# Performance work log

Hardware: AMD Instinct MI355X
Metric: run time of the kernel (lower is better)

Reference implementation:

```python
import jax, jax.numpy as jnp
import numpy as np

N = 100000   # nodes
E = 3200000  # edges per graph
DP, DA, DF, H, C = 3, 11, 32, 4, 8  # d_p, d_a, d_feat, heads, per-head dim
NEG_SLOPE = 0.2


def gat_conv(x, edge_index, W, att_src, att_dst, bias):
    """PyG GATConv with concat heads and default add_self_loops=True.
    x: [N, DF]; edge_index: [2, E] (row0=src, row1=dst); W: [DF, H*C];
    att_src/att_dst: [H, C]; bias: [H*C]. Returns [N, H*C]."""
    n = x.shape[0]
    loops = jnp.arange(n, dtype=edge_index.dtype)
    src = jnp.concatenate([edge_index[0], loops])
    dst = jnp.concatenate([edge_index[1], loops])
    h = (x @ W).reshape(n, H, C)                       # [N,H,C]
    a_s = jnp.sum(h * att_src[None], axis=-1)          # [N,H]
    a_d = jnp.sum(h * att_dst[None], axis=-1)          # [N,H]
    e = jax.nn.leaky_relu(a_s[src] + a_d[dst], NEG_SLOPE)  # [Etot,H]
    m = jax.ops.segment_max(e, dst, num_segments=n)        # stable softmax per dst
    ex = jnp.exp(e - m[dst])
    den = jax.ops.segment_sum(ex, dst, num_segments=n)
    alpha = ex / den[dst]                               # [Etot,H]
    out = jax.ops.segment_sum(h[src] * alpha[..., None], dst, num_segments=n)
    return out.reshape(n, H * C) + bias


def setup_inputs() -> dict:
    key = jax.random.key(0)
    ks = jax.random.split(key, 32)
    p = lambda k, shp: (jax.random.normal(k, shp, dtype=jnp.float32) * 0.1)
    inp = {
        "F_p_raw": jax.random.normal(ks[0], (N, DP), dtype=jnp.float32),
        "F_a_raw": jax.random.normal(ks[1], (N, DA), dtype=jnp.float32),
        "edge_index_s": jax.random.randint(ks[2], (2, E), 0, N),
        "edge_index_p": jax.random.randint(ks[3], (2, E), 0, N),
        "edge_index_a": jax.random.randint(ks[4], (2, E), 0, N),
        # align linears
        "Wp": p(ks[5], (DP, DF)), "bp": p(ks[6], (DF,)),
        "Wa": p(ks[7], (DA, DF)), "ba": p(ks[8], (DF,)),
        "Ws": p(ks[9], (DP + DA, DF)), "bs": p(ks[10], (DF,)),
        # GAT params per graph
        "Wg_s": p(ks[11], (DF, H * C)), "asrc_s": p(ks[12], (H, C)), "adst_s": p(ks[13], (H, C)), "bg_s": p(ks[14], (H * C,)),
        "Wg_p": p(ks[15], (DF, H * C)), "asrc_p": p(ks[16], (H, C)), "adst_p": p(ks[17], (H, C)), "bg_p": p(ks[18], (H * C,)),
        "Wg_a": p(ks[19], (DF, H * C)), "asrc_a": p(ks[20], (H, C)), "adst_a": p(ks[21], (H, C)), "bg_a": p(ks[22], (H * C,)),
        # fuse MLP
        "W1": p(ks[23], (3 * DF, DF)), "b1": p(ks[24], (DF,)),
        "W2": p(ks[25], (DF, DF)), "b2": p(ks[26], (DF,)),
    }
    return inp


def reference(F_p_raw, F_a_raw, edge_index_s, edge_index_p, edge_index_a,
              Wp, bp, Wa, ba, Ws, bs,
              Wg_s, asrc_s, adst_s, bg_s,
              Wg_p, asrc_p, adst_p, bg_p,
              Wg_a, asrc_a, adst_a, bg_a,
              W1, b1, W2, b2):
    f_s = jnp.concatenate([F_p_raw, F_a_raw], axis=-1) @ Ws + bs
    f_p = F_p_raw @ Wp + bp
    f_a = F_a_raw @ Wa + ba
    h_s = jax.nn.elu(gat_conv(f_s, edge_index_s, Wg_s, asrc_s, adst_s, bg_s))
    h_p = jax.nn.elu(gat_conv(f_p, edge_index_p, Wg_p, asrc_p, adst_p, bg_p))
    h_a = jax.nn.elu(gat_conv(f_a, edge_index_a, Wg_a, asrc_a, adst_a, bg_a))
    h = jnp.concatenate([h_s, h_p, h_a], axis=-1)
    h = jax.nn.relu(h @ W1 + b1)
    return h @ W2 + b2
```

## Files before the change

### kernel.cpp

```cpp
#include <hip/hip_runtime.h>
#include <hip/hip_bf16.h>
#include <stdint.h>

typedef __hip_bfloat16 bf16;

__device__ __forceinline__ float b2f(bf16 v){ return __bfloat162float(v); }

__device__ __forceinline__ uint16_t f2b(float x){
  uint32_t u = __float_as_uint(x);
  return (uint16_t)((u + 0x7FFFu + ((u >> 16) & 1u)) >> 16);
}

#define DSTS_PER_BKT 128
#define BKT_SHIFT 7
#define CAP 6144
#define BIN_IT 32
#define MAXB 1024
#define ROWS_PER_WAVE (DSTS_PER_BKT / 4)
#define CURPAD 16

struct CvtTab {
  const void* src[24];
  int n[24];
  int off[24];
};

__global__ __launch_bounds__(256) void k_detect(const void* __restrict__ sample,
                                                int* __restrict__ flag)
{
  __shared__ int bad;
  if (threadIdx.x == 0) bad = 0;
  __syncthreads();
  const unsigned short* u = (const unsigned short*)sample;
  int lbad = 0;
  for (int k = threadIdx.x; k < 1024; k += 256) {
    unsigned short b = u[k];
    unsigned e = (b >> 7) & 0xFFu;
    if (e >= 141u || (e <= 90u && (b & 0x7FFFu) != 0)) lbad = 1;
  }
  if (lbad) atomicOr(&bad, 1);
  __syncthreads();
  if (threadIdx.x == 0) flag[0] = (bad == 0) ? 1 : 0;
}

__global__ __launch_bounds__(256) void k_convert(CvtTab tab, const int* __restrict__ flag,
                                                 float* __restrict__ dst, int total)
{
  const bool isb = (*flag) != 0;
  for (int t = blockIdx.x * 256 + threadIdx.x; t < total; t += gridDim.x * 256) {
    int a = 0;
    while (a < 23 && t >= tab.off[a] + tab.n[a]) ++a;
    int j = t - tab.off[a];
    float v = isb ? b2f(((const bf16*)tab.src[a])[j])
                  : ((const float*)tab.src[a])[j];
    dst[t] = v;
  }
}

__global__ __launch_bounds__(256) void k_node(
  const float* __restrict__ cFp, const float* __restrict__ cFa,
  const float* __restrict__ cWp, const float* __restrict__ cbp,
  const float* __restrict__ cWa, const float* __restrict__ cba,
  const float* __restrict__ cWs, const float* __restrict__ cbs,
  const float* __restrict__ cWg0, const float* __restrict__ cAs0, const float* __restrict__ cAd0,
  const float* __restrict__ cWg1, const float* __restrict__ cAs1, const float* __restrict__ cAd1,
  const float* __restrict__ cWg2, const float* __restrict__ cAs2, const float* __restrict__ cAd2,
  uint32_t* __restrict__ hgb, uint16_t* __restrict__ asb, float* __restrict__ a_d,
  float* __restrict__ den, float* __restrict__ agg, int N)
{
  __shared__ float sWs[14*32];
  __shared__ float sWp[3*32];
  __shared__ float sWa[11*32];
  __shared__ float sb[3][32];
  __shared__ float sWg[3][32*32];
  __shared__ float sA[3][2][32];
  const int tid = threadIdx.x;
  for (int t = tid; t < 14*32; t += 256) sWs[t] = cWs[t];
  for (int t = tid; t < 3*32;  t += 256) sWp[t] = cWp[t];
  for (int t = tid; t < 11*32; t += 256) sWa[t] = cWa[t];
  if (tid < 32) {
    sb[0][tid] = cbs[tid]; sb[1][tid] = cbp[tid]; sb[2][tid] = cba[tid];
    sA[0][0][tid] = cAs0[tid]; sA[0][1][tid] = cAd0[tid];
    sA[1][0][tid] = cAs1[tid]; sA[1][1][tid] = cAd1[tid];
    sA[2][0][tid] = cAs2[tid]; sA[2][1][tid] = cAd2[tid];
  }
  for (int t = tid; t < 32*32; t += 256) {
    sWg[0][t] = cWg0[t]; sWg[1][t] = cWg1[t]; sWg[2][t] = cWg2[t];
  }
  __syncthreads();

  const int i = blockIdx.x * 256 + tid;
  if (i >= N) return;

  float xp[3], xa[11];
  #pragma unroll
  for (int k = 0; k < 3; ++k)  xp[k] = cFp[i*3 + k];
  #pragma unroll
  for (int k = 0; k < 11; ++k) xa[k] = cFa[i*11 + k];

  for (int g = 0; g < 3; ++g) {
    float f[32];
    if (g == 0) {
      #pragma unroll
      for (int j = 0; j < 32; ++j) {
        float acc = sb[0][j];
        #pragma unroll
        for (int k = 0; k < 3; ++k)  acc += xp[k] * sWs[k*32 + j];
        #pragma unroll
        for (int k = 0; k < 11; ++k) acc += xa[k] * sWs[(3+k)*32 + j];
        f[j] = acc;
      }
    } else if (g == 1) {
      #pragma unroll
      for (int j = 0; j < 32; ++j) {
        float acc = sb[1][j];
        #pragma unroll
        for (int k = 0; k < 3; ++k) acc += xp[k] * sWp[k*32 + j];
        f[j] = acc;
      }
    } else {
      #pragma unroll
      for (int j = 0; j < 32; ++j) {
        float acc = sb[2][j];
        #pragma unroll
        for (int k = 0; k < 11; ++k) acc += xa[k] * sWa[k*32 + j];
        f[j] = acc;
      }
    }

    const float* Wg = sWg[g];
    float hv[32];
    #pragma unroll
    for (int j = 0; j < 32; ++j) {
      float acc = 0.f;
      #pragma unroll
      for (int k = 0; k < 32; ++k) acc += f[k] * Wg[k*32 + j];
      hv[j] = acc;
    }

    float asv[4], adv[4], exv[4];
    #pragma unroll
    for (int h = 0; h < 4; ++h) {
      float s0 = 0.f, s1 = 0.f;
      #pragma unroll
      for (int c = 0; c < 8; ++c) {
        s0 += hv[h*8 + c] * sA[g][0][h*8 + c];
        s1 += hv[h*8 + c] * sA[g][1][h*8 + c];
      }
      asv[h] = s0; adv[h] = s1;
      float e = s0 + s1;
      e = e > 0.f ? e : 0.2f * e;
      exv[h] = __expf(e);
    }

    const size_t row = (size_t)g * N + i;
    uint32_t* hp = hgb + row * 16;
    #pragma unroll
    for (int q = 0; q < 4; ++q) {
      uint4 u;
      u.x = (uint32_t)f2b(hv[q*8+0]) | ((uint32_t)f2b(hv[q*8+1]) << 16);
      u.y = (uint32_t)f2b(hv[q*8+2]) | ((uint32_t)f2b(hv[q*8+3]) << 16);
      u.z = (uint32_t)f2b(hv[q*8+4]) | ((uint32_t)f2b(hv[q*8+5]) << 16);
      u.w = (uint32_t)f2b(hv[q*8+6]) | ((uint32_t)f2b(hv[q*8+7]) << 16);
      *(uint4*)(hp + q*4) = u;
    }
    *(ushort4*)(asb + row * 4) =
        make_ushort4(f2b(asv[0]), f2b(asv[1]), f2b(asv[2]), f2b(asv[3]));

    float4* agp = (float4*)(agg + row * 32);
    #pragma unroll
    for (int q = 0; q < 8; ++q) {
      float ex = exv[q >> 1];
      agp[q] = make_float4(ex*hv[q*4+0], ex*hv[q*4+1], ex*hv[q*4+2], ex*hv[q*4+3]);
    }
    *(float4*)(a_d + row*4) = make_float4(adv[0], adv[1], adv[2], adv[3]);
    *(float4*)(den + row*4) = make_float4(exv[0], exv[1], exv[2], exv[3]);
  }
}

__global__ __launch_bounds__(256) void k_hist(
  const int* __restrict__ ei0, const int* __restrict__ ei1, const int* __restrict__ ei2,
  int* __restrict__ gb_hist, int NBPG, int E)
{
  const int g = blockIdx.y;
  const int* __restrict__ ei = (g == 0) ? ei0 : (g == 1 ? ei1 : ei2);
  __shared__ int hist[MAXB];
  for (int t = threadIdx.x; t < NBPG; t += 256) hist[t] = 0;
  __syncthreads();
  const int base = blockIdx.x * (256 * BIN_IT);
  #pragma unroll
  for (int k = 0; k < BIN_IT; ++k) {
    int idx = base + k * 256 + threadIdx.x;
    if (idx < E) atomicAdd(&hist[ei[E + idx] >> BKT_SHIFT], 1);
  }
  __syncthreads();
  for (int t = threadIdx.x; t < NBPG; t += 256)
    if (hist[t]) atomicAdd(&gb_hist[g * NBPG + t], hist[t]);
}

#define SCAN_IPT 16
__global__ __launch_bounds__(256) void k_bscan(
  const int* __restrict__ gb_hist, int* __restrict__ boff, int* __restrict__ cur, int nb)
{
  __shared__ int s[256];
  const int base = threadIdx.x * SCAN_IPT;
  int v[SCAN_IPT]; int sum = 0;
  #pragma unroll
  for (int k = 0; k < SCAN_IPT; ++k) {
    int i = base + k; int x = (i < nb) ? gb_hist[i] : 0; v[k] = x; sum += x;
  }
  s[threadIdx.x] = sum;
  __syncthreads();
  for (int d = 1; d < 256; d <<= 1) {
    int t = (threadIdx.x >= d) ? s[threadIdx.x - d] : 0;
    __syncthreads();
    s[threadIdx.x] += t;
    __syncthreads();
  }
  int run = s[threadIdx.x] - sum;
  #pragma unroll
  for (int k = 0; k < SCAN_IPT; ++k) {
    int i = base + k;
    if (i < nb) { boff[i] = run; cur[(size_t)i * CURPAD] = run; run += v[k]; }
  }
  if (threadIdx.x == 255) boff[nb] = s[255];
}

__global__ __launch_bounds__(256) void k_bin(
  const int* __restrict__ ei0, const int* __restrict__ ei1, const int* __restrict__ ei2,
  int* __restrict__ cur, int* __restrict__ bins, int NBPG, int E)
{
  const int g = blockIdx.y;
  const int* __restrict__ ei = (g == 0) ? ei0 : (g == 1 ? ei1 : ei2);
  __shared__ int sp[256 * BIN_IT];
  __shared__ int hist[MAXB];
  __shared__ int soff[MAXB];
  __shared__ int grun[MAXB];
  __shared__ int s[256];
  const int tid = threadIdx.x;
  for (int t = tid; t < NBPG; t += 256) hist[t] = 0;
  __syncthreads();
  const int base = blockIdx.x * (256 * BIN_IT);

  int pk[BIN_IT];
  #pragma unroll
  for (int k = 0; k < BIN_IT; ++k) {
    int idx = base + k * 256 + tid;
    if (idx < E) {
      int d = ei[E + idx];
      int b = d >> BKT_SHIFT;
      int loc = atomicAdd(&hist[b], 1);
      pk[k] = (b << 20) | (loc << 7) | (d & (DSTS_PER_BKT - 1));
    } else pk[k] = -1;
  }
  __syncthreads();

  {
    const int sbase = tid * 4;
    int v[4]; int sum = 0;
    #pragma unroll
    for (int j = 0; j < 4; ++j) {
      int i = sbase + j; int x = (i < NBPG) ? hist[i] : 0; v[j] = x; sum += x;
    }
    s[tid] = sum;
    __syncthreads();
    for (int d = 1; d < 256; d <<= 1) {
      int t = (tid >= d) ? s[tid - d] : 0;
      __syncthreads();
      s[tid] += t;
      __syncthreads();
    }
    int run = s[tid] - sum;
    #pragma unroll
    for (int j = 0; j < 4; ++j) {
      int i = sbase + j;
      if (i < NBPG) { soff[i] = run; run += v[j]; }
    }
  }
  for (int t = tid; t < NBPG; t += 256) {
    int c = hist[t];
    grun[t] = c ? atomicAdd(&cur[(size_t)(g * NBPG + t) * CURPAD], c) : 0;
  }
  __syncthreads();

  #pragma unroll
  for (int k = 0; k < BIN_IT; ++k) {
    int p = pk[k];
    if (p >= 0) {
      int idx = base + k * 256 + tid;
      int src = ei[idx];
      int b   = p >> 20;
      int loc = (p >> 7) & 0x1FFF;
      int dl  = p & (DSTS_PER_BKT - 1);
      sp[soff[b] + loc] = (dl << 17) | src;
    }
  }
  __syncthreads();

  const int wave = tid >> 6, lane = tid & 63;
  for (int b = wave; b < NBPG; b += 4) {
    const int c  = hist[b];
    const int gb_ = grun[b];
    const int ls = soff[b];
    for (int i = lane; i < c; i += 64)
      bins[gb_ + i] = sp[ls + i];
  }
}

__global__ __launch_bounds__(256) void k_vgather(
  const int* __restrict__ boff, const int* __restrict__ bins,
  const uint32_t* __restrict__ hgb, const uint16_t* __restrict__ asb,
  const float* __restrict__ a_d,
  float* __restrict__ den, float* __restrict__ agg, int NBPG, int N)
{
  __shared__ int sorted[CAP];
  __shared__ int soff[DSTS_PER_BKT + 1];
  __shared__ int scnt[DSTS_PER_BKT];
  __shared__ int sscan[DSTS_PER_BKT];
  const int g  = blockIdx.y;
  const int b  = blockIdx.x;
  const int gb = g * NBPG + b;
  const int s0 = boff[gb];
  const int n  = boff[gb + 1] - s0;
  const int tid = threadIdx.x;
  const int wave = tid >> 6;
  const int lane = tid & 63;
  const int sub  = lane >> 4;
  const int l16  = lane & 15;
  const int h    = l16 >> 2;
  const size_t gbase = (size_t)g * N;
  const int dst0 = b * DSTS_PER_BKT;

  for (int cbase = 0; cbase < n; cbase += CAP) {
    const int m = min(CAP, n - cbase);
    if (tid < DSTS_PER_BKT) scnt[tid] = 0;
    __syncthreads();
    for (int i = tid; i < m; i += 256)
      atomicAdd(&scnt[(bins[s0 + cbase + i] >> 17) & (DSTS_PER_BKT - 1)], 1);
    __syncthreads();
    if (tid < DSTS_PER_BKT) sscan[tid] = scnt[tid];
    __syncthreads();
    for (int d = 1; d < DSTS_PER_BKT; d <<= 1) {
      int t = 0;
      if (tid < DSTS_PER_BKT && tid >= d) t = sscan[tid - d];
      __syncthreads();
      if (tid < DSTS_PER_BKT) sscan[tid] += t;
      __syncthreads();
    }
    if (tid < DSTS_PER_BKT) {
      int ex = sscan[tid] - scnt[tid];
      soff[tid] = ex;
      scnt[tid] = ex;
    }
    if (tid == 0) soff[DSTS_PER_BKT] = m;
    __syncthreads();
    for (int i = tid; i < m; i += 256) {
      int p = bins[s0 + cbase + i];
      int pos = atomicAdd(&scnt[(p >> 17) & (DSTS_PER_BKT - 1)], 1);
      sorted[pos] = p & 0x1FFFF;
    }
    __syncthreads();

    const int rbeg = wave * ROWS_PER_WAVE;
    for (int rl = rbeg; rl < rbeg + ROWS_PER_WAVE; ++rl) {
      const int dst = dst0 + rl;
      if (dst >= N) break;
      const int cs = soff[rl], ce = soff[rl + 1];
      const size_t row = gbase + dst;
      const float ad = a_d[row * 4 + h];
      float ax = 0.f, ay = 0.f, w = 0.f;
      for (int c = cs + sub; c < ce; c += 16) {
        const int i0 = c        < ce ? sorted[c]      : -1;
        const int i1 = (c + 4)  < ce ? sorted[c + 4]  : -1;
        const int i2 = (c + 8)  < ce ? sorted[c + 8]  : -1;
        const int i3 = (c + 12) < ce ? sorted[c + 12] : -1;
        const int p0 = i0 < 0 ? 0 : i0;
        const int p1 = i1 < 0 ? 0 : i1;
        const int p2 = i2 < 0 ? 0 : i2;
        const int p3 = i3 < 0 ? 0 : i3;
        const uint32_t u0 = hgb[(gbase + p0) * 16 + l16];
        const uint32_t u1 = hgb[(gbase + p1) * 16 + l16];
        const uint32_t u2 = hgb[(gbase + p2) * 16 + l16];
        const uint32_t u3 = hgb[(gbase + p3) * 16 + l16];
        const uint16_t t0 = asb[(gbase + p0) * 4 + h];
        const uint16_t t1 = asb[(gbase + p1) * 4 + h];
        const uint16_t t2 = asb[(gbase + p2) * 4 + h];
        const uint16_t t3 = asb[(gbase + p3) * 4 + h];
        float e0 = __uint_as_float((uint32_t)t0 << 16) + ad; e0 = e0 > 0.f ? e0 : 0.2f * e0;
        float e1 = __uint_as_float((uint32_t)t1 << 16) + ad; e1 = e1 > 0.f ? e1 : 0.2f * e1;
        float e2 = __uint_as_float((uint32_t)t2 << 16) + ad; e2 = e2 > 0.f ? e2 : 0.2f * e2;
        float e3 = __uint_as_float((uint32_t)t3 << 16) + ad; e3 = e3 > 0.f ? e3 : 0.2f * e3;
        const float w0 = i0 >= 0 ? __expf(e0) : 0.f;
        const float w1 = i1 >= 0 ? __expf(e1) : 0.f;
        const float w2 = i2 >= 0 ? __expf(e2) : 0.f;
        const float w3 = i3 >= 0 ? __expf(e3) : 0.f;
        ax += w0 * __uint_as_float(u0 << 16);
        ay += w0 * __uint_as_float(u0 & 0xFFFF0000u);
        ax += w1 * __uint_as_float(u1 << 16);
        ay += w1 * __uint_as_float(u1 & 0xFFFF0000u);
        ax += w2 * __uint_as_float(u2 << 16);
        ay += w2 * __uint_as_float(u2 & 0xFFFF0000u);
        ax += w3 * __uint_as_float(u3 << 16);
        ay += w3 * __uint_as_float(u3 & 0xFFFF0000u);
        w += w0 + w1 + w2 + w3;
      }
      ax += __shfl_xor(ax, 16); ay += __shfl_xor(ay, 16); w += __shfl_xor(w, 16);
      ax += __shfl_xor(ax, 32); ay += __shfl_xor(ay, 32); w += __shfl_xor(w, 32);
      if (sub == 0) {
        float2* ap = (float2*)(agg + row * 32) + l16;
        float2 sv = *ap;
        sv.x += ax; sv.y += ay;
        *ap = sv;
        if ((l16 & 3) == 0) den[row * 4 + h] += w;
      }
    }
    __syncthreads();
  }
}

__global__ __launch_bounds__(256) void k_final(
  const float* __restrict__ den, const float* __restrict__ agg,
  const float* __restrict__ cbg0, const float* __restrict__ cbg1, const float* __restrict__ cbg2,
  const float* __restrict__ cW1, const float* __restrict__ cb1,
  const float* __restrict__ cW2, const float* __restrict__ cb2,
  const int* __restrict__ flag, void* __restrict__ out, int N)
{
  __shared__ float sW1[96*32];
  __shared__ float sW2[32*32];
  __shared__ float sb1[32], sb2[32], sbg[3][32];
  const int tid = threadIdx.x;
  for (int t = tid; t < 96*32; t += 256) sW1[t] = cW1[t];
  for (int t = tid; t < 32*32; t += 256) sW2[t] = cW2[t];
  if (tid < 32) {
    sb1[tid] = cb1[tid]; sb2[tid] = cb2[tid];
    sbg[0][tid] = cbg0[tid]; sbg[1][tid] = cbg1[tid]; sbg[2][tid] = cbg2[tid];
  }
  __syncthreads();

  const int i = blockIdx.x * 256 + tid;
  if (i >= N) return;

  float h96[96];
  #pragma unroll
  for (int g = 0; g < 3; ++g) {
    const size_t row = (size_t)g * N + i;
    float4 d4 = *(const float4*)(den + row * 4);
    float invs[4] = {1.f/d4.x, 1.f/d4.y, 1.f/d4.z, 1.f/d4.w};
    const float4* av = (const float4*)(agg + row * 32);
    #pragma unroll
    for (int q = 0; q < 8; ++q) {
      float4 a4 = av[q];
      float iv = invs[q >> 1];
      float vals[4] = {a4.x, a4.y, a4.z, a4.w};
      #pragma unroll
      for (int k = 0; k < 4; ++k) {
        float v = vals[k] * iv + sbg[g][q*4 + k];
        v = v > 0.f ? v : (__expf(v) - 1.f);
        h96[g*32 + q*4 + k] = v;
      }
    }
  }

  float h1[32];
  #pragma unroll
  for (int j = 0; j < 32; ++j) {
    float acc = sb1[j];
    #pragma unroll
    for (int k = 0; k < 96; ++k) acc += h96[k] * sW1[k*32 + j];
    h1[j] = acc > 0.f ? acc : 0.f;
  }

  const bool isb = (*flag) != 0;
  #pragma unroll
  for (int j = 0; j < 32; ++j) {
    float acc = sb2[j];
    #pragma unroll
    for (int k = 0; k < 32; ++k) acc += h1[k] * sW2[k*32 + j];
    if (isb) ((bf16*)out)[(size_t)i*32 + j] = __float2bfloat16(acc);
    else     ((float*)out)[(size_t)i*32 + j] = acc;
  }
}

extern "C" void kernel_launch(void* const* d_in, const int* in_sizes, int n_in,
                              void* d_out, int out_size, void* d_ws, size_t ws_size,
                              hipStream_t stream)
{
  const int N = in_sizes[0] / 3;
  const int E = in_sizes[2] / 2;
  const int NBPG = (N + DSTS_PER_BKT - 1) / DSTS_PER_BKT;
  const int nb = 3 * NBPG;

  float* ws  = (float*)d_ws;
  int* flag  = (int*)d_ws;
  float* cvt = ws + 64;

  static const int order[24] = {1, 0,
    5, 6, 7, 8, 9, 10,
    11, 12, 13, 14,
    15, 16, 17, 18,
    19, 20, 21, 22,
    23, 24, 25, 26};
  CvtTab tab;
  int off0 = 0;
  for (int a = 0; a < 24; ++a) {
    tab.src[a] = d_in[order[a]];
    tab.n[a]   = in_sizes[order[a]];
    tab.off[a] = off0;
    off0 += tab.n[a];
  }
  const int total = off0;

  float* P[24];
  for (int a = 0; a < 24; ++a) P[a] = cvt + tab.off[a];
  float *cFa = P[0],  *cFp = P[1];
  float *cWp = P[2],  *cbp = P[3],  *cWa = P[4],  *cba = P[5],  *cWs = P[6], *cbs = P[7];
  float *cWg0 = P[8],  *cAs0 = P[9],  *cAd0 = P[10], *cbg0 = P[11];
  float *cWg1 = P[12], *cAs1 = P[13], *cAd1 = P[14], *cbg1 = P[15];
  float *cWg2 = P[16], *cAs2 = P[17], *cAd2 = P[18], *cbg2 = P[19];
  float *cW1 = P[20], *cb1 = P[21], *cW2 = P[22], *cb2 = P[23];

  int pad = (4 - (total & 3)) & 3;
  float* big = cvt + total + pad;
  const size_t n3 = (size_t)3 * N;
  float* agg  = big;
  float* a_d  = agg + n3 * 32;
  float* den  = a_d + n3 * 4;
  uint32_t* hgb = (uint32_t*)(den + n3 * 4);
  uint16_t* asb = (uint16_t*)(hgb + n3 * 16);
  int* gb_hist = (int*)(asb + n3 * 4);
  int* boff    = gb_hist + nb;
  int* cur     = boff + nb + 1;
  int* bins    = cur + (size_t)nb * CURPAD + CURPAD;

  const int ebx = (E + 256 * BIN_IT - 1) / (256 * BIN_IT);

  k_detect<<<1, 256, 0, stream>>>(d_in[1], flag);
  k_convert<<<2048, 256, 0, stream>>>(tab, flag, cvt, total);
  k_node<<<(N + 255) / 256, 256, 0, stream>>>(
      cFp, cFa, cWp, cbp, cWa, cba, cWs, cbs,
      cWg0, cAs0, cAd0, cWg1, cAs1, cAd1, cWg2, cAs2, cAd2,
      hgb, asb, a_d, den, agg, N);

  hipMemsetAsync(gb_hist, 0, nb * sizeof(int), stream);

  dim3 ge((unsigned)ebx, 3, 1);
  k_hist<<<ge, 256, 0, stream>>>(
      (const int*)d_in[2], (const int*)d_in[3], (const int*)d_in[4], gb_hist, NBPG, E);
  k_bscan<<<1, 256, 0, stream>>>(gb_hist, boff, cur, nb);
  k_bin<<<ge, 256, 0, stream>>>(
      (const int*)d_in[2], (const int*)d_in[3], (const int*)d_in[4], cur, bins, NBPG, E);

  dim3 gg((unsigned)NBPG, 3, 1);
  k_vgather<<<gg, 256, 0, stream>>>(boff, bins, hgb, asb, a_d, den, agg, NBPG, N);

  k_final<<<(N + 255) / 256, 256, 0, stream>>>(
      den, agg, cbg0, cbg1, cbg2, cW1, cb1, cW2, cb2, flag, d_out, N);
}
```

Measured before the change: 499.4 us.

## Replace global histogram/scan binning with per-block local sort plus directory

Drops the global histogram, scan and atomic cursor passes, so no memset is needed either. Each edge block now sorts its 8192 edges by bucket in shared memory and writes them contiguously, along with a per-block offset directory. The gather kernel then reads one run per edge block for its bucket and scans the run lengths itself. This saves two launches and two passes over edges, at the cost of many small scattered reads (about 391 runs per bucket) and a larger directory in the gather kernel.

```diff
diff --git a/kernel.cpp b/kernel.cpp
--- a/kernel.cpp
+++ b/kernel.cpp
@@ -13,11 +13,12 @@
 
 #define DSTS_PER_BKT 128
 #define BKT_SHIFT 7
-#define CAP 6144
+#define CHUNKE 8192
+#define CAP 8192
 #define BIN_IT 32
 #define MAXB 1024
+#define NBLKMAX 512
 #define ROWS_PER_WAVE (DSTS_PER_BKT / 4)
-#define CURPAD 16
 
 struct CvtTab {
   const void* src[24];
@@ -178,69 +179,23 @@
   }
 }
 
-__global__ __launch_bounds__(256) void k_hist(
+__global__ __launch_bounds__(256) void k_bin2(
   const int* __restrict__ ei0, const int* __restrict__ ei1, const int* __restrict__ ei2,
-  int* __restrict__ gb_hist, int NBPG, int E)
+  int* __restrict__ dir, int* __restrict__ bins, int NBPG, int NBLK, int E)
 {
   const int g = blockIdx.y;
   const int* __restrict__ ei = (g == 0) ? ei0 : (g == 1 ? ei1 : ei2);
+  __shared__ int sp[CHUNKE];
   __shared__ int hist[MAXB];
-  for (int t = threadIdx.x; t < NBPG; t += 256) hist[t] = 0;
-  __syncthreads();
-  const int base = blockIdx.x * (256 * BIN_IT);
-  #pragma unroll
-  for (int k = 0; k < BIN_IT; ++k) {
-    int idx = base + k * 256 + threadIdx.x;
-    if (idx < E) atomicAdd(&hist[ei[E + idx] >> BKT_SHIFT], 1);
-  }
-  __syncthreads();
-  for (int t = threadIdx.x; t < NBPG; t += 256)
-    if (hist[t]) atomicAdd(&gb_hist[g * NBPG + t], hist[t]);
-}
-
-#define SCAN_IPT 16
-__global__ __launch_bounds__(256) void k_bscan(
-  const int* __restrict__ gb_hist, int* __restrict__ boff, int* __restrict__ cur, int nb)
-{
-  __shared__ int s[256];
-  const int base = threadIdx.x * SCAN_IPT;
-  int v[SCAN_IPT]; int sum = 0;
-  #pragma unroll
-  for (int k = 0; k < SCAN_IPT; ++k) {
-    int i = base + k; int x = (i < nb) ? gb_hist[i] : 0; v[k] = x; sum += x;
-  }
-  s[threadIdx.x] = sum;
-  __syncthreads();
-  for (int d = 1; d < 256; d <<= 1) {
-    int t = (threadIdx.x >= d) ? s[threadIdx.x - d] : 0;
-    __syncthreads();
-    s[threadIdx.x] += t;
-    __syncthreads();
-  }
-  int run = s[threadIdx.x] - sum;
-  #pragma unroll
-  for (int k = 0; k < SCAN_IPT; ++k) {
-    int i = base + k;
-    if (i < nb) { boff[i] = run; cur[(size_t)i * CURPAD] = run; run += v[k]; }
-  }
-  if (threadIdx.x == 255) boff[nb] = s[255];
-}
-
-__global__ __launch_bounds__(256) void k_bin(
-  const int* __restrict__ ei0, const int* __restrict__ ei1, const int* __restrict__ ei2,
-  int* __restrict__ cur, int* __restrict__ bins, int NBPG, int E)
-{
-  const int g = blockIdx.y;
-  const int* __restrict__ ei = (g == 0) ? ei0 : (g == 1 ? ei1 : ei2);
-  __shared__ int sp[256 * BIN_IT];
-  __shared__ int hist[MAXB];
-  __shared__ int soff[MAXB];
-  __shared__ int grun[MAXB];
+  __shared__ int soff[MAXB + 1];
   __shared__ int s[256];
   const int tid = threadIdx.x;
+  const int blk = blockIdx.x;
+  const int base = blk * CHUNKE;
+  const int m = min(CHUNKE, E - base);
+
   for (int t = tid; t < NBPG; t += 256) hist[t] = 0;
   __syncthreads();
-  const int base = blockIdx.x * (256 * BIN_IT);
 
   int pk[BIN_IT];
   #pragma unroll
@@ -256,11 +211,11 @@
   __syncthreads();
 
   {
-    const int sbase = tid * 4;
+    const int sb = tid * 4;
     int v[4]; int sum = 0;
     #pragma unroll
     for (int j = 0; j < 4; ++j) {
-      int i = sbase + j; int x = (i < NBPG) ? hist[i] : 0; v[j] = x; sum += x;
+      int i = sb + j; int x = (i < NBPG) ? hist[i] : 0; v[j] = x; sum += x;
     }
     s[tid] = sum;
     __syncthreads();
@@ -273,15 +228,15 @@
     int run = s[tid] - sum;
     #pragma unroll
     for (int j = 0; j < 4; ++j) {
-      int i = sbase + j;
+      int i = sb + j;
       if (i < NBPG) { soff[i] = run; run += v[j]; }
     }
-  }
-  for (int t = tid; t < NBPG; t += 256) {
-    int c = hist[t];
-    grun[t] = c ? atomicAdd(&cur[(size_t)(g * NBPG + t) * CURPAD], c) : 0;
-  }
-  __syncthreads();
+    if (tid == 255) soff[NBPG] = s[255];
+  }
+  __syncthreads();
+
+  for (int t = tid; t <= NBPG; t += 256)
+    dir[((size_t)(g * (NBPG + 1) + t)) * NBLK + blk] = soff[t];
 
   #pragma unroll
   for (int k = 0; k < BIN_IT; ++k) {
@@ -297,32 +252,25 @@
   }
   __syncthreads();
 
-  const int wave = tid >> 6, lane = tid & 63;
-  for (int b = wave; b < NBPG; b += 4) {
-    const int c  = hist[b];
-    const int gb_ = grun[b];
-    const int ls = soff[b];
-    for (int i = lane; i < c; i += 64)
-      bins[gb_ + i] = sp[ls + i];
-  }
+  const size_t ob = ((size_t)(g * NBLK + blk)) << 13;
+  for (int i = tid; i < m; i += 256) bins[ob + i] = sp[i];
 }
 
 __global__ __launch_bounds__(256) void k_vgather(
-  const int* __restrict__ boff, const int* __restrict__ bins,
+  const int* __restrict__ dir, const int* __restrict__ bins,
   const uint32_t* __restrict__ hgb, const uint16_t* __restrict__ asb,
   const float* __restrict__ a_d,
-  float* __restrict__ den, float* __restrict__ agg, int NBPG, int N)
+  float* __restrict__ den, float* __restrict__ agg, int NBPG, int NBLK, int N)
 {
   __shared__ int sorted[CAP];
+  __shared__ int runbase[NBLKMAX];
+  __shared__ int pbase[NBLKMAX + 1];
   __shared__ int soff[DSTS_PER_BKT + 1];
   __shared__ int scnt[DSTS_PER_BKT];
   __shared__ int sscan[DSTS_PER_BKT];
-  const int g  = blockIdx.y;
-  const int b  = blockIdx.x;
-  const int gb = g * NBPG + b;
-  const int s0 = boff[gb];
-  const int n  = boff[gb + 1] - s0;
-  const int tid = threadIdx.x;
+  __shared__ int s[256];
+  __shared__ int schunk;
+  const int g = blockIdx.y, b = blockIdx.x, tid = threadIdx.x;
   const int wave = tid >> 6;
   const int lane = tid & 63;
   const int sub  = lane >> 4;
@@ -331,12 +279,56 @@
   const size_t gbase = (size_t)g * N;
   const int dst0 = b * DSTS_PER_BKT;
 
-  for (int cbase = 0; cbase < n; cbase += CAP) {
-    const int m = min(CAP, n - cbase);
+  const int* d0 = dir + ((size_t)(g * (NBPG + 1) + b)) * NBLK;
+  const int* d1 = d0 + NBLK;
+  for (int t = tid; t < NBLK; t += 256) {
+    int r0 = d0[t], r1 = d1[t];
+    runbase[t] = ((g * NBLK + t) << 13) + r0;
+    pbase[t] = r1 - r0;
+  }
+  __syncthreads();
+  {
+    int v0 = (2*tid     < NBLK) ? pbase[2*tid]     : 0;
+    int v1 = (2*tid + 1 < NBLK) ? pbase[2*tid + 1] : 0;
+    __syncthreads();
+    int sum = v0 + v1; s[tid] = sum;
+    __syncthreads();
+    for (int d = 1; d < 256; d <<= 1) {
+      int t = (tid >= d) ? s[tid - d] : 0;
+      __syncthreads();
+      s[tid] += t;
+      __syncthreads();
+    }
+    int run = s[tid] - sum;
+    if (2*tid     <= NBLK) pbase[2*tid]     = run;
+    if (2*tid + 1 <= NBLK) pbase[2*tid + 1] = run + v0;
+  }
+  __syncthreads();
+  const int ntot = pbase[NBLK];
+
+  int rlo = 0;
+  while (rlo < NBLK) {
+    if (tid == 0) {
+      if (rlo == 0 && ntot <= CAP) schunk = NBLK;
+      else {
+        int lim = pbase[rlo] + CAP;
+        int hi = rlo + 1;
+        while (hi < NBLK && pbase[hi + 1] <= lim) ++hi;
+        schunk = hi;
+      }
+    }
+    __syncthreads();
+    const int rhi = schunk;
+    const int m = pbase[rhi] - pbase[rlo];
+
     if (tid < DSTS_PER_BKT) scnt[tid] = 0;
     __syncthreads();
-    for (int i = tid; i < m; i += 256)
-      atomicAdd(&scnt[(bins[s0 + cbase + i] >> 17) & (DSTS_PER_BKT - 1)], 1);
+    for (int rr = rlo + wave * 4 + (lane >> 4); rr < rhi; rr += 16) {
+      const int l = pbase[rr + 1] - pbase[rr];
+      const int gbb = runbase[rr];
+      for (int i = (lane & 15); i < l; i += 16)
+        atomicAdd(&scnt[(bins[gbb + i] >> 17) & (DSTS_PER_BKT - 1)], 1);
+    }
     __syncthreads();
     if (tid < DSTS_PER_BKT) sscan[tid] = scnt[tid];
     __syncthreads();
@@ -354,10 +346,14 @@
     }
     if (tid == 0) soff[DSTS_PER_BKT] = m;
     __syncthreads();
-    for (int i = tid; i < m; i += 256) {
-      int p = bins[s0 + cbase + i];
-      int pos = atomicAdd(&scnt[(p >> 17) & (DSTS_PER_BKT - 1)], 1);
-      sorted[pos] = p & 0x1FFFF;
+    for (int rr = rlo + wave * 4 + (lane >> 4); rr < rhi; rr += 16) {
+      const int l = pbase[rr + 1] - pbase[rr];
+      const int gbb = runbase[rr];
+      for (int i = (lane & 15); i < l; i += 16) {
+        int p = bins[gbb + i];
+        int pos = atomicAdd(&scnt[(p >> 17) & (DSTS_PER_BKT - 1)], 1);
+        sorted[pos] = p & 0x1FFFF;
+      }
     }
     __syncthreads();
 
@@ -415,6 +411,7 @@
       }
     }
     __syncthreads();
+    rlo = rhi;
   }
 }
 
@@ -488,7 +485,7 @@
   const int N = in_sizes[0] / 3;
   const int E = in_sizes[2] / 2;
   const int NBPG = (N + DSTS_PER_BKT - 1) / DSTS_PER_BKT;
-  const int nb = 3 * NBPG;
+  const int NBLK = (E + CHUNKE - 1) / CHUNKE;
 
   float* ws  = (float*)d_ws;
   int* flag  = (int*)d_ws;
@@ -527,12 +524,8 @@
   float* den  = a_d + n3 * 4;
   uint32_t* hgb = (uint32_t*)(den + n3 * 4);
   uint16_t* asb = (uint16_t*)(hgb + n3 * 16);
-  int* gb_hist = (int*)(asb + n3 * 4);
-  int* boff    = gb_hist + nb;
-  int* cur     = boff + nb + 1;
-  int* bins    = cur + (size_t)nb * CURPAD + CURPAD;
-
-  const int ebx = (E + 256 * BIN_IT - 1) / (256 * BIN_IT);
+  int* dir  = (int*)(asb + n3 * 4);
+  int* bins = dir + (size_t)3 * (NBPG + 1) * NBLK;
 
   k_detect<<<1, 256, 0, stream>>>(d_in[1], flag);
   k_convert<<<2048, 256, 0, stream>>>(tab, flag, cvt, total);
@@ -541,17 +534,13 @@
       cWg0, cAs0, cAd0, cWg1, cAs1, cAd1, cWg2, cAs2, cAd2,
       hgb, asb, a_d, den, agg, N);
 
-  hipMemsetAsync(gb_hist, 0, nb * sizeof(int), stream);
-
-  dim3 ge((unsigned)ebx, 3, 1);
-  k_hist<<<ge, 256, 0, stream>>>(
-      (const int*)d_in[2], (const int*)d_in[3], (const int*)d_in[4], gb_hist, NBPG, E);
-  k_bscan<<<1, 256, 0, stream>>>(gb_hist, boff, cur, nb);
-  k_bin<<<ge, 256, 0, stream>>>(
-      (const int*)d_in[2], (const int*)d_in[3], (const int*)d_in[4], cur, bins, NBPG, E);
+  dim3 gbk((unsigned)NBLK, 3, 1);
+  k_bin2<<<gbk, 256, 0, stream>>>(
+      (const int*)d_in[2], (const int*)d_in[3], (const int*)d_in[4],
+      dir, bins, NBPG, NBLK, E);
 
   dim3 gg((unsigned)NBPG, 3, 1);
-  k_vgather<<<gg, 256, 0, stream>>>(boff, bins, hgb, asb, a_d, den, agg, NBPG, N);
+  k_vgather<<<gg, 256, 0, stream>>>(dir, bins, hgb, asb, a_d, den, agg, NBPG, NBLK, N);
 
   k_final<<<(N + 255) / 256, 256, 0, stream>>>(
       den, agg, cbg0, cbg1, cbg2, cW1, cb1, cW2, cb2, flag, d_out, N);
```

Result: faster. 462.0 us (-7.5%).
